# Kernel optimization log

Measured on AMD Instinct MI355X. Metric: run time of the kernel, lower is better.

## Reference

```python
import jax, jax.numpy as jnp
import numpy as np

N_NODES = 50000
N_EDGES = 800000
IN_FEATS, HIDDEN_FEATS, NUM_CLASSES = 64, 64, 32


def setup_inputs() -> dict:
    key = jax.random.key(0)
    ks = jax.random.split(key, 9)
    features = jax.random.normal(ks[0], (N_NODES, IN_FEATS), dtype=jnp.float32)
    src = jax.random.randint(ks[1], (N_EDGES,), 0, N_NODES, dtype=jnp.int32)
    dst = jax.random.randint(ks[2], (N_EDGES,), 0, N_NODES, dtype=jnp.int32)
    def lin(k, fan_in, fan_out):
        bound = 1.0 / np.sqrt(fan_in)
        return jax.random.uniform(k, (fan_in, fan_out), jnp.float32, -bound, bound)
    W_self1 = lin(ks[3], IN_FEATS, HIDDEN_FEATS)
    W_neigh1 = lin(ks[4], IN_FEATS, HIDDEN_FEATS)
    b1 = jnp.zeros((HIDDEN_FEATS,), jnp.float32)
    W_self2 = lin(ks[5], HIDDEN_FEATS, NUM_CLASSES)
    W_neigh2 = lin(ks[6], HIDDEN_FEATS, NUM_CLASSES)
    b2 = jnp.zeros((NUM_CLASSES,), jnp.float32)
    return {"features": features, "W_self1": W_self1, "W_neigh1": W_neigh1, "b1": b1,
            "W_self2": W_self2, "W_neigh2": W_neigh2, "b2": b2, "src": src, "dst": dst}


def _sage_mean(x, W_self, W_neigh, b, src, dst, n_nodes):
    # mean over in-neighbors: edge (u, v) sends x[u] into v
    agg = jax.ops.segment_sum(x[src], dst, num_segments=n_nodes)          # [N, F]
    deg = jax.ops.segment_sum(jnp.ones((src.shape[0],), x.dtype), dst,
                              num_segments=n_nodes)                        # [N]
    h_neigh = agg / jnp.maximum(deg, 1.0)[:, None]                         # zero-in-degree -> 0
    return x @ W_self + h_neigh @ W_neigh + b


def reference(features, W_self1, W_neigh1, b1, W_self2, W_neigh2, b2, src, dst):
    n = features.shape[0]
    h = jax.nn.relu(_sage_mean(features, W_self1, W_neigh1, b1, src, dst, n))
    return _sage_mean(h, W_self2, W_neigh2, b2, src, dst, n)
```

## Files before the change

kernel.cpp:

```cpp
#include <hip/hip_runtime.h>

#define N_NODES 50000
#define N_EDGES 800000
#define NB 196
#define PBLOCKS 256
#define CHUNK 3125
#define GEMM_BLOCKS 782

typedef unsigned short ushort_t;
typedef __attribute__((ext_vector_type(8))) short bf16x8;
typedef __attribute__((ext_vector_type(4))) float f32x4;


__device__ __forceinline__ float bflo(unsigned int u) {
    return __uint_as_float(u << 16);
}
__device__ __forceinline__ float bfhi(unsigned int u) {
    return __uint_as_float(u & 0xffff0000u);
}
__device__ __forceinline__ ushort_t f2bf(float f) {
    unsigned int x = __float_as_uint(f);
    return (ushort_t)((x + 0x7fffu + ((x >> 16) & 1u)) >> 16);
}
__device__ __forceinline__ unsigned int pack_bf(float lo, float hi) {
    return (unsigned int)f2bf(lo) | ((unsigned int)f2bf(hi) << 16);
}
__device__ __forceinline__ void split_bf(float v, short& hi, short& lo) {
    ushort_t h = f2bf(v);
    float r = v - __uint_as_float((unsigned int)h << 16);
    hi = (short)h;
    lo = (short)f2bf(r);
}

__global__ __launch_bounds__(256)
void gemm128_and_count(const float* __restrict__ A,
                       const float* __restrict__ B1,
                       const float* __restrict__ B2,
                       ushort_t* __restrict__ Cself,
                       ushort_t* __restrict__ Cn,
                       const int* __restrict__ dst,
                       int* __restrict__ blocktot) {
    __shared__ int hist[NB];

    if (blockIdx.x >= GEMM_BLOCKS) {
        const int pb = blockIdx.x - GEMM_BLOCKS;
        for (int i = threadIdx.x; i < NB; i += 256) hist[i] = 0;
        __syncthreads();
        const int e0 = pb * CHUNK;
        const int e1 = e0 + CHUNK;
        for (int e = e0 + (int)threadIdx.x; e < e1; e += 256)
            atomicAdd(&hist[dst[e] >> 8], 1);
        __syncthreads();
        for (int i = threadIdx.x; i < NB; i += 256)
            blocktot[i * PBLOCKS + pb] = hist[i];
        return;
    }

    const int l  = threadIdx.x & 63;
    const int w  = threadIdx.x >> 6;
    const int lr = l & 15;
    const int lk = (l >> 4) << 3;

    bf16x8 bhi[2][2], blo[2][2];
#pragma unroll
    for (int nt = 0; nt < 2; ++nt) {
        const int n = w * 32 + nt * 16 + lr;
        const float* Bp = (n < 64) ? (B1 + n) : (B2 + (n - 64));
#pragma unroll
        for (int ks = 0; ks < 2; ++ks) {
#pragma unroll
            for (int j = 0; j < 8; ++j) {
                float bv = Bp[(size_t)(ks * 32 + lk + j) * 64];
                short h, lo;
                split_bf(bv, h, lo);
                bhi[nt][ks][j] = h;
                blo[nt][ks][j] = lo;
            }
        }
    }

    const int m0 = blockIdx.x * 64;
    f32x4 acc[4][2];
#pragma unroll
    for (int mt = 0; mt < 4; ++mt)
#pragma unroll
        for (int nt = 0; nt < 2; ++nt) {
            f32x4 z = {0.f, 0.f, 0.f, 0.f};
            acc[mt][nt] = z;
        }

#pragma unroll
    for (int mt = 0; mt < 4; ++mt) {
        const int m = m0 + mt * 16 + lr;
        const bool valid = (m < N_NODES);
        const float* Ap = A + (size_t)m * 64 + lk;
#pragma unroll
        for (int ks = 0; ks < 2; ++ks) {
            float4 f0, f1;
            if (valid) {
                f0 = *(const float4*)(Ap + ks * 32);
                f1 = *(const float4*)(Ap + ks * 32 + 4);
            } else {
                f0 = make_float4(0.f, 0.f, 0.f, 0.f);
                f1 = f0;
            }
            const float fv[8] = {f0.x, f0.y, f0.z, f0.w, f1.x, f1.y, f1.z, f1.w};
            bf16x8 ahi, alo;
#pragma unroll
            for (int j = 0; j < 8; ++j) {
                short h, lo;
                split_bf(fv[j], h, lo);
                ahi[j] = h;
                alo[j] = lo;
            }
#pragma unroll
            for (int nt = 0; nt < 2; ++nt) {
                acc[mt][nt] = __builtin_amdgcn_mfma_f32_16x16x32_bf16(
                    ahi, bhi[nt][ks], acc[mt][nt], 0, 0, 0);
                acc[mt][nt] = __builtin_amdgcn_mfma_f32_16x16x32_bf16(
                    alo, bhi[nt][ks], acc[mt][nt], 0, 0, 0);
                acc[mt][nt] = __builtin_amdgcn_mfma_f32_16x16x32_bf16(
                    ahi, blo[nt][ks], acc[mt][nt], 0, 0, 0);
            }
        }
    }

#pragma unroll
    for (int mt = 0; mt < 4; ++mt) {
        const int mbase = m0 + mt * 16 + ((l >> 4) << 2);
#pragma unroll
        for (int nt = 0; nt < 2; ++nt) {
            const int n = w * 32 + nt * 16 + lr;
            ushort_t* T = (n < 64) ? (Cself + n) : (Cn + (n - 64));
#pragma unroll
            for (int r = 0; r < 4; ++r) {
                const int m = mbase + r;
                if (m < N_NODES) T[(size_t)m * 64] = f2bf(acc[mt][nt][r]);
            }
        }
    }
}

__global__ __launch_bounds__(256)
void part_write(const int* __restrict__ src, const int* __restrict__ dst,
                const int* __restrict__ blocktot, unsigned int* __restrict__ brec) {
    __shared__ int ssum[256];
    __shared__ int cur[NB];
    const int pb = blockIdx.x;
    const int t  = threadIdx.x;

    int rsum = 0, mypart = 0;
    if (t < NB) {
        const int* rp = blocktot + t * PBLOCKS;
#pragma unroll 8
        for (int j = 0; j < PBLOCKS; ++j) {
            if (j == pb) mypart = rsum;
            rsum += rp[j];
        }
    }
    ssum[t] = (t < NB) ? rsum : 0;
    __syncthreads();
    for (int off = 1; off < 256; off <<= 1) {
        int add = (t >= off) ? ssum[t - off] : 0;
        __syncthreads();
        ssum[t] += add;
        __syncthreads();
    }
    if (t < NB) cur[t] = (ssum[t] - rsum) + mypart;
    __syncthreads();

    const int e0 = pb * CHUNK;
    const int e1 = e0 + CHUNK;
    for (int e = e0 + t; e < e1; e += 256) {
        int d = dst[e];
        int s = src[e];
        int pos = atomicAdd(&cur[d >> 8], 1);
        brec[pos] = ((unsigned int)(d & 255) << 16) | (unsigned int)s;
    }
}

__global__ __launch_bounds__(256)
void bucket_fill(const int* __restrict__ blocktot,
                 const unsigned int* __restrict__ brec,
                 int* __restrict__ csr_src, int* __restrict__ row_ptr) {
    __shared__ int ssum[256];
    __shared__ int cnt[256];
    __shared__ int cur[256];
    const int b = blockIdx.x;
    const int node0 = b * 256;
    const int t = threadIdx.x;

    int rsum = 0;
    if (t < NB) {
        const int* rp = blocktot + t * PBLOCKS;
#pragma unroll 8
        for (int j = 0; j < PBLOCKS; ++j) rsum += rp[j];
    }
    ssum[t] = (t < NB) ? rsum : 0;
    __syncthreads();
    for (int off = 1; off < 256; off <<= 1) {
        int add = (t >= off) ? ssum[t - off] : 0;
        __syncthreads();
        ssum[t] += add;
        __syncthreads();
    }
    const int w0 = (b == 0) ? 0 : ssum[b - 1];
    const int w1 = ssum[b];
    __syncthreads();

    cnt[t] = 0;
    __syncthreads();
    for (int i = w0 + t; i < w1; i += 256)
        atomicAdd(&cnt[brec[i] >> 16], 1);
    __syncthreads();
    const int v = cnt[t];
    cur[t] = v;
    __syncthreads();
    for (int off = 1; off < 256; off <<= 1) {
        int add = (t >= off) ? cur[t - off] : 0;
        __syncthreads();
        cur[t] += add;
        __syncthreads();
    }
    const int excl = cur[t] - v;
    const int node = node0 + t;
    if (node <= N_NODES) row_ptr[node] = w0 + excl;
    __syncthreads();
    cur[t] = w0 + excl;
    __syncthreads();
    for (int i = w0 + t; i < w1; i += 256) {
        unsigned int r = brec[i];
        int pos = atomicAdd(&cur[r >> 16], 1);
        csr_src[pos] = (int)(r & 0xffffu);
    }
}

__global__ __launch_bounds__(256)
void gemm_cat64_bf16(const ushort_t* __restrict__ A,
                     const float* __restrict__ B1,
                     const float* __restrict__ B2,
                     ushort_t* __restrict__ Cself,
                     ushort_t* __restrict__ Cn) {
    const int l  = threadIdx.x & 63;
    const int w  = threadIdx.x >> 6;
    const int lr = l & 15;
    const int lk = (l >> 4) << 3;

    const int n = w * 16 + lr;
    const float* Bp = (n < 32) ? (B1 + n) : (B2 + (n - 32));
    bf16x8 bhi[2], blo[2];
#pragma unroll
    for (int ks = 0; ks < 2; ++ks) {
#pragma unroll
        for (int j = 0; j < 8; ++j) {
            float bv = Bp[(size_t)(ks * 32 + lk + j) * 32];
            short h, lo;
            split_bf(bv, h, lo);
            bhi[ks][j] = h;
            blo[ks][j] = lo;
        }
    }

    const int m0 = blockIdx.x * 64;
    f32x4 acc[4];
#pragma unroll
    for (int mt = 0; mt < 4; ++mt) {
        f32x4 z = {0.f, 0.f, 0.f, 0.f};
        acc[mt] = z;
    }

#pragma unroll
    for (int mt = 0; mt < 4; ++mt) {
        const int m = m0 + mt * 16 + lr;
        const bool valid = (m < N_NODES);
#pragma unroll
        for (int ks = 0; ks < 2; ++ks) {
            bf16x8 a;
            if (valid) {
                a = *(const bf16x8*)&A[(size_t)m * 64 + ks * 32 + lk];
            } else {
                bf16x8 z = {0, 0, 0, 0, 0, 0, 0, 0};
                a = z;
            }
            acc[mt] = __builtin_amdgcn_mfma_f32_16x16x32_bf16(a, bhi[ks], acc[mt], 0, 0, 0);
            acc[mt] = __builtin_amdgcn_mfma_f32_16x16x32_bf16(a, blo[ks], acc[mt], 0, 0, 0);
        }
    }

    ushort_t* T = (n < 32) ? (Cself + n) : (Cn + (n - 32));
#pragma unroll
    for (int mt = 0; mt < 4; ++mt) {
        const int mbase = m0 + mt * 16 + ((l >> 4) << 2);
#pragma unroll
        for (int r = 0; r < 4; ++r) {
            const int m = mbase + r;
            if (m < N_NODES) T[(size_t)m * 32] = f2bf(acc[mt][r]);
        }
    }
}

__global__ __launch_bounds__(256)
void gather1(const ushort_t* __restrict__ Tself,
             const ushort_t* __restrict__ Tn,
             const int* __restrict__ row_ptr,
             const int* __restrict__ csr_src, const float* __restrict__ bias,
             ushort_t* __restrict__ out) {
    constexpr int F = 64;
    constexpr int LPR = 8;
    constexpr int G = 4;
    constexpr int MAXJ = 8;
    const int lane = threadIdx.x & 63;
    const int half = lane >> 5;
    const int hl   = lane & 31;
    const int r = hl / LPR;
    const int c = hl % LPR;
    const int v = (((int)blockIdx.x * (int)blockDim.x + (int)threadIdx.x) >> 6) * 2 + half;
    if (v >= N_NODES) return;
    const int start = row_ptr[v];
    const int cnt   = row_ptr[v + 1] - start;

    float a[8];
#pragma unroll
    for (int i = 0; i < 8; ++i) a[i] = 0.f;

#define ACC8(u)                                           \
    a[0] += bflo(u.x); a[1] += bfhi(u.x);                 \
    a[2] += bflo(u.y); a[3] += bfhi(u.y);                 \
    a[4] += bflo(u.z); a[5] += bfhi(u.z);                 \
    a[6] += bflo(u.w); a[7] += bfhi(u.w);

    int idx = 0;
    if (hl < cnt) idx = csr_src[start + hl];

    const int nfast = (cnt < 32) ? cnt : 32;
    int  sidx[MAXJ];
    bool act[MAXJ];
#pragma unroll
    for (int j = 0; j < MAXJ; ++j) {
        const int t = r + j * G;
        act[j]  = (t < nfast);
        sidx[j] = __shfl(idx, half * 32 + t);
    }
    uint4 u[MAXJ];
#pragma unroll
    for (int j = 0; j < MAXJ; ++j) {
        u[j] = make_uint4(0u, 0u, 0u, 0u);
        if (act[j]) u[j] = *(const uint4*)&Tn[(size_t)sidx[j] * F + c * 8];
    }
#pragma unroll
    for (int j = 0; j < MAXJ; ++j) { ACC8(u[j]) }

    for (int t = 32 + r; t < cnt; t += G) {
        const int s = csr_src[start + t];
        uint4 uu = *(const uint4*)&Tn[(size_t)s * F + c * 8];
        ACC8(uu)
    }
#undef ACC8

#pragma unroll
    for (int off = LPR; off < 32; off <<= 1) {
#pragma unroll
        for (int i = 0; i < 8; ++i) a[i] += __shfl_xor(a[i], off);
    }

    if (r == 0) {
        const float inv = 1.0f / (float)max(cnt, 1);
        uint4 su = *(const uint4*)&Tself[(size_t)v * F + c * 8];
        float4 bA = *(const float4*)&bias[c * 8];
        float4 bB = *(const float4*)&bias[c * 8 + 4];
        float o[8];
        o[0] = bflo(su.x) + a[0] * inv + bA.x;
        o[1] = bfhi(su.x) + a[1] * inv + bA.y;
        o[2] = bflo(su.y) + a[2] * inv + bA.z;
        o[3] = bfhi(su.y) + a[3] * inv + bA.w;
        o[4] = bflo(su.z) + a[4] * inv + bB.x;
        o[5] = bfhi(su.z) + a[5] * inv + bB.y;
        o[6] = bflo(su.w) + a[6] * inv + bB.z;
        o[7] = bfhi(su.w) + a[7] * inv + bB.w;
#pragma unroll
        for (int i = 0; i < 8; ++i) o[i] = fmaxf(o[i], 0.f);
        uint4 p;
        p.x = pack_bf(o[0], o[1]); p.y = pack_bf(o[2], o[3]);
        p.z = pack_bf(o[4], o[5]); p.w = pack_bf(o[6], o[7]);
        *(uint4*)&out[(size_t)v * F + c * 8] = p;
    }
}

__global__ __launch_bounds__(256)
void gather2(const ushort_t* __restrict__ Tself,
             const ushort_t* __restrict__ Tn,
             const int* __restrict__ row_ptr,
             const int* __restrict__ csr_src, const float* __restrict__ bias,
             float* __restrict__ out) {
    constexpr int F = 32;
    constexpr int LPR = 4;
    constexpr int G = 4;
    constexpr int MAXJ = 8;
    const int lane = threadIdx.x & 63;
    const int q  = lane >> 4;
    const int hl = lane & 15;
    const int r = hl >> 2;
    const int c = hl & 3;
    const int v = (((int)blockIdx.x * (int)blockDim.x + (int)threadIdx.x) >> 6) * 4 + q;
    if (v >= N_NODES) return;
    const int start = row_ptr[v];
    const int cnt   = row_ptr[v + 1] - start;

    float a[8];
#pragma unroll
    for (int i = 0; i < 8; ++i) a[i] = 0.f;

#define ACC8(u)                                           \
    a[0] += bflo(u.x); a[1] += bfhi(u.x);                 \
    a[2] += bflo(u.y); a[3] += bfhi(u.y);                 \
    a[4] += bflo(u.z); a[5] += bfhi(u.z);                 \
    a[6] += bflo(u.w); a[7] += bfhi(u.w);

    int idx0 = 0, idx1 = 0;
    if (hl < cnt)      idx0 = csr_src[start + hl];
    if (16 + hl < cnt) idx1 = csr_src[start + 16 + hl];

    const int nfast = (cnt < 32) ? cnt : 32;
    int  sidx[MAXJ];
    bool act[MAXJ];
#pragma unroll
    for (int j = 0; j < MAXJ; ++j) {
        const int t = r + j * G;
        act[j] = (t < nfast);
        sidx[j] = (j < 4) ? __shfl(idx0, q * 16 + t)
                          : __shfl(idx1, q * 16 + (t - 16));
    }
    uint4 u[MAXJ];
#pragma unroll
    for (int j = 0; j < MAXJ; ++j) {
        u[j] = make_uint4(0u, 0u, 0u, 0u);
        if (act[j]) u[j] = *(const uint4*)&Tn[(size_t)sidx[j] * F + c * 8];
    }
#pragma unroll
    for (int j = 0; j < MAXJ; ++j) { ACC8(u[j]) }

    for (int t = 32 + r; t < cnt; t += G) {
        const int s = csr_src[start + t];
        uint4 uu = *(const uint4*)&Tn[(size_t)s * F + c * 8];
        ACC8(uu)
    }
#undef ACC8

#pragma unroll
    for (int off = LPR; off < 16; off <<= 1) {
#pragma unroll
        for (int i = 0; i < 8; ++i) a[i] += __shfl_xor(a[i], off);
    }

    if (r == 0) {
        const float inv = 1.0f / (float)max(cnt, 1);
        uint4 su = *(const uint4*)&Tself[(size_t)v * F + c * 8];
        float4 bA = *(const float4*)&bias[c * 8];
        float4 bB = *(const float4*)&bias[c * 8 + 4];
        float o[8];
        o[0] = bflo(su.x) + a[0] * inv + bA.x;
        o[1] = bfhi(su.x) + a[1] * inv + bA.y;
        o[2] = bflo(su.y) + a[2] * inv + bA.z;
        o[3] = bfhi(su.y) + a[3] * inv + bA.w;
        o[4] = bflo(su.z) + a[4] * inv + bB.x;
        o[5] = bfhi(su.z) + a[5] * inv + bB.y;
        o[6] = bflo(su.w) + a[6] * inv + bB.z;
        o[7] = bfhi(su.w) + a[7] * inv + bB.w;
        *(float4*)&out[(size_t)v * F + c * 8]     = make_float4(o[0], o[1], o[2], o[3]);
        *(float4*)&out[(size_t)v * F + c * 8 + 4] = make_float4(o[4], o[5], o[6], o[7]);
    }
}

extern "C" void kernel_launch(void* const* d_in, const int* in_sizes, int n_in,
                              void* d_out, int out_size, void* d_ws, size_t ws_size,
                              hipStream_t stream) {
    const float* features = (const float*)d_in[0];
    const float* W_self1  = (const float*)d_in[1];
    const float* W_neigh1 = (const float*)d_in[2];
    const float* b1       = (const float*)d_in[3];
    const float* W_self2  = (const float*)d_in[4];
    const float* W_neigh2 = (const float*)d_in[5];
    const float* b2       = (const float*)d_in[6];
    const int*   src      = (const int*)d_in[7];
    const int*   dst      = (const int*)d_in[8];

    ushort_t* Tself1 = (ushort_t*)d_ws;
    ushort_t* Tn1    = Tself1 + (size_t)N_NODES * 64;
    ushort_t* h      = Tn1 + (size_t)N_NODES * 64;
    int* row_ptr     = (int*)(h + (size_t)N_NODES * 64);
    int* csr_src     = row_ptr + (N_NODES + 1);
    unsigned int* brec = (unsigned int*)(csr_src + N_EDGES);
    int* blocktot    = (int*)(brec + N_EDGES);

    ushort_t* Tself2 = Tself1;
    ushort_t* Tn2    = Tself1 + (size_t)N_NODES * 32;

    gemm128_and_count<<<GEMM_BLOCKS + PBLOCKS, 256, 0, stream>>>(
        features, W_self1, W_neigh1, Tself1, Tn1, dst, blocktot);
    part_write<<<PBLOCKS, 256, 0, stream>>>(src, dst, blocktot, brec);
    bucket_fill<<<NB, 256, 0, stream>>>(blocktot, brec, csr_src, row_ptr);
    gather1<<<(N_NODES + 7) / 8, 256, 0, stream>>>(
        Tself1, Tn1, row_ptr, csr_src, b1, h);
    gemm_cat64_bf16<<<GEMM_BLOCKS, 256, 0, stream>>>(h, W_self2, W_neigh2, Tself2, Tn2);
    gather2<<<(N_NODES + 15) / 16, 256, 0, stream>>>(
        Tself2, Tn2, row_ptr, csr_src, b2, (float*)d_out);
}
```

Baseline: 161.2 us.

## Fuse CSR bucket fill with layer-1 gather, staging CSR indices in LDS

Merges the bucket_fill CSR construction kernel with the first-layer neighbor gather into one 1024-thread-per-bucket kernel. Source indices for each bucket are kept in shared memory so the gather reads them from LDS instead of global memory, and one launch is removed. In exchange, the gather runs on only 196 blocks, which reduces parallelism and latency hiding for the random feature loads.

```diff
diff --git a/kernel.cpp b/kernel.cpp
--- a/kernel.cpp
+++ b/kernel.cpp
@@ -6,6 +6,7 @@
 #define PBLOCKS 256
 #define CHUNK 3125
 #define GEMM_BLOCKS 782
+#define CSR_CAP 4608
 
 typedef unsigned short ushort_t;
 typedef __attribute__((ext_vector_type(8))) short bf16x8;
@@ -179,60 +180,159 @@
     }
 }
 
-__global__ __launch_bounds__(256)
-void bucket_fill(const int* __restrict__ blocktot,
+__global__ __launch_bounds__(1024)
+void csr_gather1(const int* __restrict__ blocktot,
                  const unsigned int* __restrict__ brec,
-                 int* __restrict__ csr_src, int* __restrict__ row_ptr) {
+                 int* __restrict__ csr_src, int* __restrict__ row_ptr,
+                 const ushort_t* __restrict__ Tself,
+                 const ushort_t* __restrict__ Tn,
+                 const float* __restrict__ bias,
+                 ushort_t* __restrict__ out) {
     __shared__ int ssum[256];
     __shared__ int cnt[256];
+    __shared__ int rs[256];
     __shared__ int cur[256];
+    __shared__ int csr_lds[CSR_CAP];
+
     const int b = blockIdx.x;
     const int node0 = b * 256;
     const int t = threadIdx.x;
 
-    int rsum = 0;
-    if (t < NB) {
-        const int* rp = blocktot + t * PBLOCKS;
+    if (t < 256) {
+        int rsum = 0;
+        if (t < NB) {
+            const int* rp = blocktot + t * PBLOCKS;
 #pragma unroll 8
-        for (int j = 0; j < PBLOCKS; ++j) rsum += rp[j];
-    }
-    ssum[t] = (t < NB) ? rsum : 0;
+            for (int j = 0; j < PBLOCKS; ++j) rsum += rp[j];
+        }
+        ssum[t] = rsum;
+        cnt[t] = 0;
+    }
     __syncthreads();
     for (int off = 1; off < 256; off <<= 1) {
-        int add = (t >= off) ? ssum[t - off] : 0;
-        __syncthreads();
-        ssum[t] += add;
+        int add = (t < 256 && t >= off) ? ssum[t - off] : 0;
+        __syncthreads();
+        if (t < 256) ssum[t] += add;
         __syncthreads();
     }
     const int w0 = (b == 0) ? 0 : ssum[b - 1];
     const int w1 = ssum[b];
     __syncthreads();
 
-    cnt[t] = 0;
-    __syncthreads();
-    for (int i = w0 + t; i < w1; i += 256)
+    for (int i = w0 + t; i < w1; i += 1024)
         atomicAdd(&cnt[brec[i] >> 16], 1);
     __syncthreads();
-    const int v = cnt[t];
-    cur[t] = v;
+
+    if (t < 256) cur[t] = cnt[t];
     __syncthreads();
     for (int off = 1; off < 256; off <<= 1) {
-        int add = (t >= off) ? cur[t - off] : 0;
-        __syncthreads();
-        cur[t] += add;
-        __syncthreads();
-    }
-    const int excl = cur[t] - v;
-    const int node = node0 + t;
-    if (node <= N_NODES) row_ptr[node] = w0 + excl;
-    __syncthreads();
-    cur[t] = w0 + excl;
-    __syncthreads();
-    for (int i = w0 + t; i < w1; i += 256) {
-        unsigned int r = brec[i];
-        int pos = atomicAdd(&cur[r >> 16], 1);
-        csr_src[pos] = (int)(r & 0xffffu);
-    }
+        int add = (t < 256 && t >= off) ? cur[t - off] : 0;
+        __syncthreads();
+        if (t < 256) cur[t] += add;
+        __syncthreads();
+    }
+    if (t < 256) {
+        const int excl = cur[t] - cnt[t];
+        rs[t] = excl;
+        const int node = node0 + t;
+        if (node <= N_NODES) row_ptr[node] = w0 + excl;
+    }
+    __syncthreads();
+    if (t < 256) cur[t] = rs[t];
+    __syncthreads();
+
+    for (int i = w0 + t; i < w1; i += 1024) {
+        const unsigned int r = brec[i];
+        const int pos = atomicAdd(&cur[r >> 16], 1);
+        const int s = (int)(r & 0xffffu);
+        csr_src[w0 + pos] = s;
+        if (pos < CSR_CAP) csr_lds[pos] = s;
+    }
+    __syncthreads();
+
+    const int wv   = t >> 6;
+    const int lane = t & 63;
+    const int half = lane >> 5;
+    const int hl   = lane & 31;
+    const int r = hl >> 3;
+    const int c = hl & 7;
+
+#define ACC8(u)                                           \
+    a[0] += bflo(u.x); a[1] += bfhi(u.x);                 \
+    a[2] += bflo(u.y); a[3] += bfhi(u.y);                 \
+    a[4] += bflo(u.z); a[5] += bfhi(u.z);                 \
+    a[6] += bflo(u.w); a[7] += bfhi(u.w);
+
+    for (int it = 0; it < 8; ++it) {
+        const int pair = wv + (it << 4);
+        const int dloc = (pair << 1) + half;
+        const int v = node0 + dloc;
+        if (v >= N_NODES) continue;
+        const int sl = rs[dloc];
+        const int cn = cnt[dloc];
+
+        float a[8];
+#pragma unroll
+        for (int i = 0; i < 8; ++i) a[i] = 0.f;
+
+        const int nfast = (cn < 32) ? cn : 32;
+        int  sidx[8];
+        bool act[8];
+#pragma unroll
+        for (int j = 0; j < 8; ++j) {
+            const int tt = r + (j << 2);
+            act[j] = (tt < nfast);
+            sidx[j] = 0;
+            if (act[j]) {
+                const int ad = sl + tt;
+                sidx[j] = (ad < CSR_CAP) ? csr_lds[ad] : csr_src[w0 + ad];
+            }
+        }
+        uint4 u[8];
+#pragma unroll
+        for (int j = 0; j < 8; ++j) {
+            u[j] = make_uint4(0u, 0u, 0u, 0u);
+            if (act[j]) u[j] = *(const uint4*)&Tn[(size_t)sidx[j] * 64 + c * 8];
+        }
+#pragma unroll
+        for (int j = 0; j < 8; ++j) { ACC8(u[j]) }
+
+        for (int tt = 32 + r; tt < cn; tt += 4) {
+            const int ad = sl + tt;
+            const int s = (ad < CSR_CAP) ? csr_lds[ad] : csr_src[w0 + ad];
+            const uint4 uu = *(const uint4*)&Tn[(size_t)s * 64 + c * 8];
+            ACC8(uu)
+        }
+
+#pragma unroll
+        for (int off = 8; off < 32; off <<= 1) {
+#pragma unroll
+            for (int i = 0; i < 8; ++i) a[i] += __shfl_xor(a[i], off);
+        }
+
+        if (r == 0) {
+            const float inv = 1.0f / (float)max(cn, 1);
+            uint4 su = *(const uint4*)&Tself[(size_t)v * 64 + c * 8];
+            float4 bA = *(const float4*)&bias[c * 8];
+            float4 bB = *(const float4*)&bias[c * 8 + 4];
+            float o[8];
+            o[0] = bflo(su.x) + a[0] * inv + bA.x;
+            o[1] = bfhi(su.x) + a[1] * inv + bA.y;
+            o[2] = bflo(su.y) + a[2] * inv + bA.z;
+            o[3] = bfhi(su.y) + a[3] * inv + bA.w;
+            o[4] = bflo(su.z) + a[4] * inv + bB.x;
+            o[5] = bfhi(su.z) + a[5] * inv + bB.y;
+            o[6] = bflo(su.w) + a[6] * inv + bB.z;
+            o[7] = bfhi(su.w) + a[7] * inv + bB.w;
+#pragma unroll
+            for (int i = 0; i < 8; ++i) o[i] = fmaxf(o[i], 0.f);
+            uint4 p;
+            p.x = pack_bf(o[0], o[1]); p.y = pack_bf(o[2], o[3]);
+            p.z = pack_bf(o[4], o[5]); p.w = pack_bf(o[6], o[7]);
+            *(uint4*)&out[(size_t)v * 64 + c * 8] = p;
+        }
+    }
+#undef ACC8
 }
 
 __global__ __launch_bounds__(256)
@@ -296,93 +396,6 @@
             const int m = mbase + r;
             if (m < N_NODES) T[(size_t)m * 32] = f2bf(acc[mt][r]);
         }
-    }
-}
-
-__global__ __launch_bounds__(256)
-void gather1(const ushort_t* __restrict__ Tself,
-             const ushort_t* __restrict__ Tn,
-             const int* __restrict__ row_ptr,
-             const int* __restrict__ csr_src, const float* __restrict__ bias,
-             ushort_t* __restrict__ out) {
-    constexpr int F = 64;
-    constexpr int LPR = 8;
-    constexpr int G = 4;
-    constexpr int MAXJ = 8;
-    const int lane = threadIdx.x & 63;
-    const int half = lane >> 5;
-    const int hl   = lane & 31;
-    const int r = hl / LPR;
-    const int c = hl % LPR;
-    const int v = (((int)blockIdx.x * (int)blockDim.x + (int)threadIdx.x) >> 6) * 2 + half;
-    if (v >= N_NODES) return;
-    const int start = row_ptr[v];
-    const int cnt   = row_ptr[v + 1] - start;
-
-    float a[8];
-#pragma unroll
-    for (int i = 0; i < 8; ++i) a[i] = 0.f;
-
-#define ACC8(u)                                           \
-    a[0] += bflo(u.x); a[1] += bfhi(u.x);                 \
-    a[2] += bflo(u.y); a[3] += bfhi(u.y);                 \
-    a[4] += bflo(u.z); a[5] += bfhi(u.z);                 \
-    a[6] += bflo(u.w); a[7] += bfhi(u.w);
-
-    int idx = 0;
-    if (hl < cnt) idx = csr_src[start + hl];
-
-    const int nfast = (cnt < 32) ? cnt : 32;
-    int  sidx[MAXJ];
-    bool act[MAXJ];
-#pragma unroll
-    for (int j = 0; j < MAXJ; ++j) {
-        const int t = r + j * G;
-        act[j]  = (t < nfast);
-        sidx[j] = __shfl(idx, half * 32 + t);
-    }
-    uint4 u[MAXJ];
-#pragma unroll
-    for (int j = 0; j < MAXJ; ++j) {
-        u[j] = make_uint4(0u, 0u, 0u, 0u);
-        if (act[j]) u[j] = *(const uint4*)&Tn[(size_t)sidx[j] * F + c * 8];
-    }
-#pragma unroll
-    for (int j = 0; j < MAXJ; ++j) { ACC8(u[j]) }
-
-    for (int t = 32 + r; t < cnt; t += G) {
-        const int s = csr_src[start + t];
-        uint4 uu = *(const uint4*)&Tn[(size_t)s * F + c * 8];
-        ACC8(uu)
-    }
-#undef ACC8
-
-#pragma unroll
-    for (int off = LPR; off < 32; off <<= 1) {
-#pragma unroll
-        for (int i = 0; i < 8; ++i) a[i] += __shfl_xor(a[i], off);
-    }
-
-    if (r == 0) {
-        const float inv = 1.0f / (float)max(cnt, 1);
-        uint4 su = *(const uint4*)&Tself[(size_t)v * F + c * 8];
-        float4 bA = *(const float4*)&bias[c * 8];
-        float4 bB = *(const float4*)&bias[c * 8 + 4];
-        float o[8];
-        o[0] = bflo(su.x) + a[0] * inv + bA.x;
-        o[1] = bfhi(su.x) + a[1] * inv + bA.y;
-        o[2] = bflo(su.y) + a[2] * inv + bA.z;
-        o[3] = bfhi(su.y) + a[3] * inv + bA.w;
-        o[4] = bflo(su.z) + a[4] * inv + bB.x;
-        o[5] = bfhi(su.z) + a[5] * inv + bB.y;
-        o[6] = bflo(su.w) + a[6] * inv + bB.z;
-        o[7] = bfhi(su.w) + a[7] * inv + bB.w;
-#pragma unroll
-        for (int i = 0; i < 8; ++i) o[i] = fmaxf(o[i], 0.f);
-        uint4 p;
-        p.x = pack_bf(o[0], o[1]); p.y = pack_bf(o[2], o[3]);
-        p.z = pack_bf(o[4], o[5]); p.w = pack_bf(o[6], o[7]);
-        *(uint4*)&out[(size_t)v * F + c * 8] = p;
     }
 }
 
@@ -498,9 +511,8 @@
     gemm128_and_count<<<GEMM_BLOCKS + PBLOCKS, 256, 0, stream>>>(
         features, W_self1, W_neigh1, Tself1, Tn1, dst, blocktot);
     part_write<<<PBLOCKS, 256, 0, stream>>>(src, dst, blocktot, brec);
-    bucket_fill<<<NB, 256, 0, stream>>>(blocktot, brec, csr_src, row_ptr);
-    gather1<<<(N_NODES + 7) / 8, 256, 0, stream>>>(
-        Tself1, Tn1, row_ptr, csr_src, b1, h);
+    csr_gather1<<<NB, 1024, 0, stream>>>(
+        blocktot, brec, csr_src, row_ptr, Tself1, Tn1, b1, h);
     gemm_cat64_bf16<<<GEMM_BLOCKS, 256, 0, stream>>>(h, W_self2, W_neigh2, Tself2, Tn2);
     gather2<<<(N_NODES + 15) / 16, 256, 0, stream>>>(
         Tself2, Tn2, row_ptr, csr_src, b2, (float*)d_out);
```

New measurement: 161.3 us. Within noise of the previous version (+0.1%).
